# Kernel tuning notes

Measured on AMD Instinct MI355X. Metric: run time of the kernel, lower is better.

Reference implementation:

```python
import jax, jax.numpy as jnp
import numpy as np

D = 1024

def setup_inputs() -> dict:
    key = jax.random.key(0)
    ks = jax.random.split(key, 9)
    s = 1.0 / np.sqrt(D)
    x = jax.random.normal(ks[0], (4096, 8, D), dtype=jnp.float32)
    Wq = jax.random.uniform(ks[1], (D, D), jnp.float32, -s, s)
    bq = jax.random.uniform(ks[2], (D,), jnp.float32, -s, s)
    Wk = jax.random.uniform(ks[3], (D, D), jnp.float32, -s, s)
    bk = jax.random.uniform(ks[4], (D,), jnp.float32, -s, s)
    Wv = jax.random.uniform(ks[5], (D, D), jnp.float32, -s, s)
    bv = jax.random.uniform(ks[6], (D,), jnp.float32, -s, s)
    Wo = jax.random.uniform(ks[7], (D, D), jnp.float32, -s, s)
    bo = jax.random.uniform(ks[8], (D,), jnp.float32, -s, s)
    return {"x": x, "Wq": Wq, "bq": bq, "Wk": Wk, "bk": bk,
            "Wv": Wv, "bv": bv, "Wo": Wo, "bo": bo}

def reference(x, Wq, bq, Wk, bk, Wv, bv, Wo, bo):
    # x: (S, B, D) seq-first, matching torch module
    Q = jax.nn.elu(x @ Wq.T + bq) + 1.0  # (S,B,D)
    K = jax.nn.elu(x @ Wk.T + bk) + 1.0  # (S,B,D)
    V = x @ Wv.T + bv                    # (S,B,D)
    # KV = K^T V per batch: (B, D, D)
    KV = jnp.einsum('sbd,sbe->bde', K, V)
    # out = Q @ KV per batch, back to (S,B,D)
    out = jnp.einsum('sbd,bde->sbe', Q, KV)
    return out @ Wo.T + bo
```

## Files before the change

### kernel.cpp

```cpp
#include <hip/hip_runtime.h>


typedef __bf16 bf16;
typedef __attribute__((ext_vector_type(8))) __bf16 bf16x8;
typedef __attribute__((ext_vector_type(4))) __bf16 bf16x4;
typedef __attribute__((ext_vector_type(4))) float f32x4;

static constexpr int S = 4096;
static constexpr int B = 8;
static constexpr int D = 1024;
static constexpr int SB = S * B;
static constexpr long long NELEM = (long long)SB * D;

__device__ __forceinline__ void load_lds16(const bf16* g, void* l)
{
    __builtin_amdgcn_global_load_lds(
        (const __attribute__((address_space(1))) void*)g,
        (__attribute__((address_space(3))) void*)l, 16, 0, 0);
}

__global__ void cvt_f32_to_bf16(const float* __restrict__ in, bf16* __restrict__ out, int n)
{
    int i = (blockIdx.x * blockDim.x + threadIdx.x) * 4;
    int stride = gridDim.x * blockDim.x * 4;
    for (; i < n; i += stride) {
        float4 v = *(const float4*)(in + i);
        bf16x4 o;
        o[0] = (bf16)v.x; o[1] = (bf16)v.y; o[2] = (bf16)v.z; o[3] = (bf16)v.w;
        *(bf16x4*)(out + i) = o;
    }
}

__global__ void cvt_permute(const float* __restrict__ in, bf16* __restrict__ out)
{
    long long i = ((long long)blockIdx.x * blockDim.x + threadIdx.x) * 8;
    const long long stride = (long long)gridDim.x * blockDim.x * 8;
    for (; i < NELEM; i += stride) {
        const long long s = i >> 13;
        const long long r = i & 8191;
        const long long b = r >> 10;
        const long long d = r & 1023;
        float4 v0 = *(const float4*)(in + i);
        float4 v1 = *(const float4*)(in + i + 4);
        bf16x8 o;
        o[0] = (bf16)v0.x; o[1] = (bf16)v0.y; o[2] = (bf16)v0.z; o[3] = (bf16)v0.w;
        o[4] = (bf16)v1.x; o[5] = (bf16)v1.y; o[6] = (bf16)v1.z; o[7] = (bf16)v1.w;
        *(bf16x8*)(out + b * ((long long)S * D) + s * D + d) = o;
    }
}

__global__ __launch_bounds__(256) void cvt_transpose_1024(
    const float* __restrict__ in, bf16* __restrict__ out)
{
    __shared__ bf16 tile[64][72];
    const int e0 = blockIdx.y * 64;
    const int d0 = blockIdx.x * 64;
    const int t  = threadIdx.x;
    const int rl = t >> 3;
    const int c8 = (t & 7) * 8;
    #pragma unroll
    for (int p = 0; p < 2; ++p) {
        int r = rl + p * 32;
        float4 v0 = *(const float4*)(in + (long long)(e0 + r) * D + d0 + c8);
        float4 v1 = *(const float4*)(in + (long long)(e0 + r) * D + d0 + c8 + 4);
        tile[c8+0][r] = (bf16)v0.x; tile[c8+1][r] = (bf16)v0.y;
        tile[c8+2][r] = (bf16)v0.z; tile[c8+3][r] = (bf16)v0.w;
        tile[c8+4][r] = (bf16)v1.x; tile[c8+5][r] = (bf16)v1.y;
        tile[c8+6][r] = (bf16)v1.z; tile[c8+7][r] = (bf16)v1.w;
    }
    __syncthreads();
    #pragma unroll
    for (int p = 0; p < 2; ++p) {
        int dr = rl + p * 32;
        *(bf16x8*)(out + (long long)(d0 + dr) * D + e0 + c8) = *(bf16x8*)(&tile[dr][c8]);
    }
}

__global__ __launch_bounds__(256) void bvo_kernel(
    const float* __restrict__ Wo, const float* __restrict__ bv, float* __restrict__ bvo)
{
    const int row = blockIdx.x;
    const int t = threadIdx.x;
    float4 w = *(const float4*)(Wo + (long long)row * D + t * 4);
    float4 b = *(const float4*)(bv + t * 4);
    float s = w.x*b.x + w.y*b.y + w.z*b.z + w.w*b.w;
    __shared__ float red[256];
    red[t] = s; __syncthreads();
    for (int off = 128; off > 0; off >>= 1) {
        if (t < off) red[t] += red[t + off];
        __syncthreads();
    }
    if (t == 0) bvo[row] = red[0];
}

__global__ __launch_bounds__(256) void kv_add(const bf16* __restrict__ p, bf16* __restrict__ o)
{
    const long long DD = (long long)D * D;
    const int b = blockIdx.y;
    const long long i = ((long long)blockIdx.x * 256 + threadIdx.x) * 8;
    bf16x8 u = *(const bf16x8*)(p + (2 * b) * DD + i);
    bf16x8 v = *(const bf16x8*)(p + (2 * b + 1) * DD + i);
    bf16x8 r;
    #pragma unroll
    for (int j = 0; j < 8; ++j) r[j] = (bf16)((float)u[j] + (float)v[j]);
    *(bf16x8*)(o + b * DD + i) = r;
}

template<int BM, int BN, int WM, int WN, int EPI, int OUTF32, int BIASROW>
__global__ __launch_bounds__(WM * WN * 64, 2) void gemm_bt(
    const bf16* __restrict__ A, const bf16* __restrict__ Bm,
    const float* __restrict__ bias, void* __restrict__ Cout,
    int lda, int ldb, int ldc, int K,
    long long aBatch, long long bBatch, long long cBatch)
{
    constexpr int THREADS = WM * WN * 64;
    constexpr int WROWS = BM / WM, WCOLS = BN / WN;
    constexpr int MI = WROWS / 16, NI = WCOLS / 16;
    constexpr int ABYTES = BM * 64;
    constexpr int BBYTES = BN * 64;
    constexpr int BUF = ABYTES + BBYTES;

    __shared__ unsigned char smem[4 * BUF];

    const int tid  = threadIdx.x;
    const int lane = tid & 63;
    const int wave = tid >> 6;
    const int wr   = wave / WN;
    const int wc   = wave % WN;
    const int bz   = blockIdx.z;

    const int nx  = gridDim.x;
    const int bid = blockIdx.y * nx + blockIdx.x;
    const int cpx = (nx * gridDim.y) >> 3;
    const int swz = (bid & 7) * cpx + (bid >> 3);
    const long long m0 = (long long)(swz / nx) * BM;
    const long long n0 = (long long)(swz % nx) * BN;

    const bf16* Ab = A  + bz * aBatch + m0 * lda;
    const bf16* Bb = Bm + bz * bBatch + n0 * ldb;

    f32x4 acc[MI][NI] = {};
    const int NT = K >> 5;

    auto stage = [&](int t) {
        unsigned char* dst = smem + (t & 3) * BUF;
        const long long kk = (long long)t << 5;
        #pragma unroll
        for (int j = 0; j < 2; ++j) {
            const int g  = wave * 64 + lane + j * THREADS;
            const int gs = g ^ ((g >> 3) & 3);
            const int row = gs >> 2, col = (gs & 3) * 8;
            load_lds16(Ab + (long long)row * lda + kk + col,
                       dst + (wave * 64 + j * THREADS) * 16);
        }
        #pragma unroll
        for (int j = 0; j < 2; ++j) {
            const int g  = wave * 64 + lane + j * THREADS;
            const int gs = g ^ ((g >> 3) & 3);
            const int row = gs >> 2, col = (gs & 3) * 8;
            load_lds16(Bb + (long long)row * ldb + kk + col,
                       dst + ABYTES + (wave * 64 + j * THREADS) * 16);
        }
    };

    stage(0); stage(1); stage(2);

    const int ko2 = (lane >> 4) * 16;
    const int la15 = lane & 15;

    for (int t = 0; t < NT; ++t) {
        if (t + 2 < NT)      asm volatile("s_waitcnt vmcnt(8)" ::: "memory");
        else if (t + 1 < NT) asm volatile("s_waitcnt vmcnt(4)" ::: "memory");
        else                 asm volatile("s_waitcnt vmcnt(0)" ::: "memory");
        __builtin_amdgcn_s_barrier();
        asm volatile("" ::: "memory");

        if (t + 3 < NT) stage(t + 3);

        const unsigned char* buf = smem + (t & 3) * BUF;
        bf16x8 a[MI], b[NI];
        #pragma unroll
        for (int mi = 0; mi < MI; ++mi) {
            int ad = (wr * WROWS + mi * 16 + la15) * 64 + ko2;
            ad ^= ((ad >> 7) & 3) << 4;
            a[mi] = *(const bf16x8*)(buf + ad);
        }
        #pragma unroll
        for (int ni = 0; ni < NI; ++ni) {
            int ad = (wc * WCOLS + ni * 16 + la15) * 64 + ko2;
            ad ^= ((ad >> 7) & 3) << 4;
            b[ni] = *(const bf16x8*)(buf + ABYTES + ad);
        }

        __builtin_amdgcn_s_setprio(1);
        #pragma unroll
        for (int mi = 0; mi < MI; ++mi)
            #pragma unroll
            for (int ni = 0; ni < NI; ++ni)
                acc[mi][ni] = __builtin_amdgcn_mfma_f32_16x16x32_bf16(
                    a[mi], b[ni], acc[mi][ni], 0, 0, 0);
        __builtin_amdgcn_s_setprio(0);
    }

    const int crow = (lane >> 4) * 4;
    const int ccol = lane & 15;
    #pragma unroll
    for (int ni = 0; ni < NI; ++ni) {
        const long long c = n0 + wc * WCOLS + ni * 16 + ccol;
        float bcol = 0.0f;
        if (!BIASROW && bias) bcol = bias[c];
        #pragma unroll
        for (int mi = 0; mi < MI; ++mi) {
            const long long r0 = m0 + wr * WROWS + mi * 16 + crow;
            #pragma unroll
            for (int j = 0; j < 4; ++j) {
                float v = acc[mi][ni][j];
                v += BIASROW ? bias[r0 + j] : bcol;
                if (EPI == 1) v = (v > 0.0f) ? (v + 1.0f) : __expf(v);
                const long long idx = bz * cBatch + (r0 + j) * ldc + c;
                if (OUTF32) ((float*)Cout)[idx] = v;
                else        ((bf16*)Cout)[idx]  = (bf16)v;
            }
        }
    }
}

template<int EPI, int OUTF32, int BIASROW, int SPLITK, int GROUPN>
__global__ __launch_bounds__(512, 1) void gemm8p(
    const bf16* __restrict__ A, const bf16* __restrict__ Bm,
    const float* __restrict__ bias, void* __restrict__ Cout,
    int lda, int ldb, int ldc, int K,
    long long aBatch, long long bBatch, long long cBatch)
{
    __shared__ unsigned char smem[131072];

    const int tid  = threadIdx.x;
    const int lane = tid & 63;
    const int wave = tid >> 6;
    const int wr   = wave >> 2;
    const int wc   = wave & 3;
    const int bz    = blockIdx.z;
    const int batch = bz / SPLITK;
    const int kseg  = bz % SPLITK;

    const int nx  = gridDim.x;
    const int ny  = gridDim.y;
    const int bid = blockIdx.y * nx + blockIdx.x;
    const int cpx = (nx * ny) >> 3;
    const int swzb = (bid & 7) * cpx + (bid >> 3);
    long long m0, n0;
    if (GROUPN) { n0 = (long long)(swzb / ny) * 256; m0 = (long long)(swzb % ny) * 256; }
    else        { m0 = (long long)(swzb / nx) * 256; n0 = (long long)(swzb % nx) * 256; }

    const bf16* Ab = A  + batch * aBatch + m0 * lda + (long long)kseg * K;
    const bf16* Bb = Bm + batch * bBatch + n0 * ldb + (long long)kseg * K;

    const int sg = (lane & 3) ^ ((lane >> 3) & 3);
    const long long srow = wave * 32 + (lane >> 2);
    const bf16* srcA  = Ab + srow * lda + sg * 8;
    const bf16* srcA2 = srcA + 16 * (long long)lda;
    const bf16* srcB  = Bb + srow * ldb + sg * 8;
    const bf16* srcB2 = srcB + 16 * (long long)ldb;
    const int dstoff = wave * 2048;

    const int la15 = lane & 15;
    const int rsw  = (lane >> 4) ^ ((la15 >> 1) & 3);
    const int a16  = (wr * 128 + la15) * 4 + rsw;
    const int b16  = (wc * 64  + la15) * 4 + rsw;

    f32x4 acc[8][4] = {};
    const int NT = K >> 6;
    const int NI = NT >> 1;

    auto stageA = [&](int T, int kh) {
        const int reg = ((((T & 1) << 1) | kh) << 14);
        const long long kp = ((long long)T << 6) + (kh << 5);
        load_lds16(srcA  + kp, smem + reg + dstoff);
        load_lds16(srcA2 + kp, smem + reg + dstoff + 1024);
    };
    auto stageB = [&](int T, int kh) {
        const int reg = 65536 + ((((T & 1) << 1) | kh) << 14);
        const long long kp = ((long long)T << 6) + (kh << 5);
        load_lds16(srcB  + kp, smem + reg + dstoff);
        load_lds16(srcB2 + kp, smem + reg + dstoff + 1024);
    };

    stageB(0, 0); stageA(0, 0); stageB(0, 1); stageA(0, 1);
    stageB(1, 0); stageA(1, 0); stageB(1, 1);
    asm volatile("s_waitcnt vmcnt(6)" ::: "memory");

    bf16x8 bfr[4];
    for (int i = 0; i < NI; ++i) {
        const int t = 2 * i;
        const bool nl = (i + 1 < NI);
        #pragma unroll
        for (int p = 0; p < 8; ++p) {
            const int ks  = (p >> 1) & 1;
            const int ch  = p & 1;
            const int buf = p >> 2;
            const int regA = ((buf << 1) | ks) << 14;
            const int regB = 65536 + regA;

            __builtin_amdgcn_s_barrier();
            __builtin_amdgcn_sched_barrier(0);

            bf16x8 afr[4];
            if (ch == 0) {
                #pragma unroll
                for (int ni = 0; ni < 4; ++ni)
                    bfr[ni] = *(const bf16x8*)(smem + regB + (b16 + ni * 64) * 16);
            }
            #pragma unroll
            for (int m4 = 0; m4 < 4; ++m4)
                afr[m4] = *(const bf16x8*)(smem + regA + (a16 + (ch * 4 + m4) * 64) * 16);

            if      (p == 0) stageA(t + 1, 1);
            else if (p == 1) { if (t + 2 < NT) stageB(t + 2, 0); }
            else if (p == 2) { if (t + 2 < NT) stageA(t + 2, 0); }
            else if (p == 3) { if (t + 2 < NT) stageB(t + 2, 1); }
            else if (p == 4) { if (t + 2 < NT) stageA(t + 2, 1); }
            else if (p == 5) { if (t + 3 < NT) stageB(t + 3, 0); }
            else if (p == 6) { if (t + 3 < NT) stageA(t + 3, 0); }
            else             { if (t + 3 < NT) stageB(t + 3, 1); }

            if (p == 3) {
                if (nl) asm volatile("s_waitcnt vmcnt(6)" ::: "memory");
                else    asm volatile("s_waitcnt vmcnt(0)" ::: "memory");
            } else if (p == 7) {
                if (nl) asm volatile("s_waitcnt vmcnt(6)" ::: "memory");
            }

            __builtin_amdgcn_s_setprio(1);
            #pragma unroll
            for (int m4 = 0; m4 < 4; ++m4)
                #pragma unroll
                for (int ni = 0; ni < 4; ++ni)
                    acc[ch * 4 + m4][ni] = __builtin_amdgcn_mfma_f32_16x16x32_bf16(
                        afr[m4], bfr[ni], acc[ch * 4 + m4][ni], 0, 0, 0);
            __builtin_amdgcn_s_setprio(0);
        }
    }

    const bool doElu = (EPI == 1) || (EPI == 2 && m0 < 1024);
    const long long cb = (long long)bz * cBatch;
    const int crow = (lane >> 4) * 4;

    if constexpr (OUTF32 != 0) {
        float* lt = (float*)smem;
        #pragma unroll
        for (int q = 0; q < 4; ++q) {
            __builtin_amdgcn_s_barrier();
            __builtin_amdgcn_sched_barrier(0);
            if (wr == (q >> 1)) {
                #pragma unroll
                for (int m4 = 0; m4 < 4; ++m4) {
                    const int mi = (q & 1) * 4 + m4;
                    const int lrow = m4 * 16 + crow;
                    const long long r0 = m0 + q * 64 + lrow;
                    #pragma unroll
                    for (int ni = 0; ni < 4; ++ni) {
                        const int lcol = wc * 64 + ni * 16 + la15;
                        float bb = 0.0f;
                        if (!BIASROW && bias) bb = bias[n0 + lcol];
                        #pragma unroll
                        for (int j = 0; j < 4; ++j) {
                            float v = acc[mi][ni][j] + (BIASROW ? bias[r0 + j] : bb);
                            if (doElu) v = (v > 0.0f) ? (v + 1.0f) : __expf(v);
                            lt[(lrow + j) * 260 + lcol] = v;
                        }
                    }
                }
            }
            __builtin_amdgcn_s_barrier();
            #pragma unroll
            for (int it = 0; it < 8; ++it) {
                const int chk = it * 512 + tid;
                const int r   = chk >> 6;
                const int g   = chk & 63;
                float4 v = *(const float4*)(lt + r * 260 + g * 4);
                *(float4*)((float*)Cout + cb + (m0 + q * 64 + r) * ldc + n0 + g * 4) = v;
            }
        }
    } else {
        bf16* lt = (bf16*)smem;
        #pragma unroll
        for (int half = 0; half < 2; ++half) {
            __builtin_amdgcn_s_barrier();
            __builtin_amdgcn_sched_barrier(0);
            if (wr == half) {
                #pragma unroll
                for (int mi = 0; mi < 8; ++mi) {
                    const int lrow = mi * 16 + crow;
                    const long long r0 = m0 + half * 128 + lrow;
                    #pragma unroll
                    for (int ni = 0; ni < 4; ++ni) {
                        const int lcol = wc * 64 + ni * 16 + la15;
                        float bb = 0.0f;
                        if (!BIASROW && bias) bb = bias[n0 + lcol];
                        #pragma unroll
                        for (int j = 0; j < 4; ++j) {
                            float v = acc[mi][ni][j] + (BIASROW ? bias[r0 + j] : bb);
                            if (doElu) v = (v > 0.0f) ? (v + 1.0f) : __expf(v);
                            lt[(lrow + j) * 264 + lcol] = (bf16)v;
                        }
                    }
                }
            }
            __builtin_amdgcn_s_barrier();
            #pragma unroll
            for (int it = 0; it < 8; ++it) {
                const int chk = it * 512 + tid;
                const int m   = chk >> 5;
                const int nof = (chk & 31) * 8;
                bf16x8 v = *(const bf16x8*)(lt + m * 264 + nof);
                *(bf16x8*)((bf16*)Cout + cb + (m0 + half * 128 + m) * ldc + n0 + nof) = v;
            }
        }
    }
}

extern "C" void kernel_launch(void* const* d_in, const int* in_sizes, int n_in,
                              void* d_out, int out_size, void* d_ws, size_t ws_size,
                              hipStream_t stream)
{
    const float* x  = (const float*)d_in[0];
    const float* Wq = (const float*)d_in[1];
    const float* bq = (const float*)d_in[2];
    const float* Wk = (const float*)d_in[3];
    const float* bk = (const float*)d_in[4];
    const float* Wv = (const float*)d_in[5];
    const float* bv = (const float*)d_in[6];
    const float* Wo = (const float*)d_in[7];
    const float* bo = (const float*)d_in[8];
    float* out = (float*)d_out;

    char* ws = (char*)d_ws;
    if (ws_size < (size_t)159383552) return;
    bf16*  xbp  = (bf16*)(ws + 0);
    bf16*  part = (bf16*)(ws + 67108864);
    bf16*  Qb   = (bf16*)(ws + 67108864);
    bf16*  wvT  = (bf16*)(ws + 134217728);
    float* bkvo = (float*)(ws + 134217728 + 2097152);
    bf16*  KVo  = (bf16*)(ws + 134217728);
    bf16*  wqb  = (bf16*)(ws + 150994944);
    bf16*  wob  = wqb + 1048576;
    bf16*  wkvo = wob + 1048576;
    bf16*  KVb  = (bf16*)d_out;

    const long long SD = (long long)S * D;

    cvt_permute<<<8192, 256, 0, stream>>>(x, xbp);
    cvt_f32_to_bf16<<<1024, 256, 0, stream>>>(Wq, wqb, D * D);
    cvt_f32_to_bf16<<<1024, 256, 0, stream>>>(Wo, wob, D * D);
    cvt_f32_to_bf16<<<1024, 256, 0, stream>>>(Wk, wkvo, D * D);
    cvt_transpose_1024<<<dim3(16, 16), 256, 0, stream>>>(Wv, wvT);
    bvo_kernel<<<1024, 256, 0, stream>>>(Wo, bv, bkvo + 1024);
    hipMemcpyAsync(bkvo, bk, D * sizeof(float), hipMemcpyDeviceToDevice, stream);

    gemm_bt<128, 128, 2, 2, 0, 0, 0><<<dim3(8, 8, 1), 256, 0, stream>>>(
        wob, wvT, nullptr, wkvo + (long long)1024 * 1024, D, D, D, D, 0, 0, 0);

    gemm8p<2, 0, 1, 1, 1><<<dim3(16, 8, 8), 512, 0, stream>>>(
        wkvo, xbp, bkvo, KVb, D, D, S, D,
        0, SD, (long long)2048 * S);

    gemm8p<0, 0, 0, 2, 0><<<dim3(4, 4, 16), 512, 0, stream>>>(
        KVb + (long long)1024 * S, KVb, nullptr, part, S, S, D, 2048,
        (long long)2048 * S, (long long)2048 * S, (long long)D * D);

    kv_add<<<dim3(512, 8), 256, 0, stream>>>(part, KVo);

    gemm8p<1, 0, 0, 1, 0><<<dim3(4, 16, 8), 512, 0, stream>>>(
        xbp, wqb, bq, Qb, D, D, D, D, SD, 0, SD);

    gemm8p<0, 1, 0, 1, 0><<<dim3(4, 16, 8), 512, 0, stream>>>(
        Qb, KVo, bo, out, D, D, B * D, D,
        SD, (long long)D * D, (long long)D);
}
```

Baseline: 487.2 us.

## Add 128x128-tile GEMM kernel with two-per-CU occupancy for projection GEMMs

Adds a new 256-thread GEMM kernel with 128x128 output tiles, a double-buffered direct-to-LDS load pipeline, an XOR-swizzled LDS layout and a grouped block swizzle. It replaces the larger 512-thread gemm8p tiles in the K/V projection, Q projection and output projection, launching four times as many blocks. The aim is better occupancy (launch bounds of 2 blocks per CU) and load balance across CUs, at the cost of less operand reuse per tile and more global traffic.

```diff
diff --git a/kernel.cpp b/kernel.cpp
--- a/kernel.cpp
+++ b/kernel.cpp
@@ -419,6 +419,174 @@
     }
 }
 
+template<int EPI, int OUTF32, int BIASROW, int GROUPN>
+__global__ __launch_bounds__(256, 2) void gemm_r128(
+    const bf16* __restrict__ A, const bf16* __restrict__ Bm,
+    const float* __restrict__ bias, void* __restrict__ Cout,
+    int lda, int ldb, int ldc, int K,
+    long long aBatch, long long bBatch, long long cBatch)
+{
+    __shared__ unsigned char smem[32768];
+
+    const int tid  = threadIdx.x;
+    const int lane = tid & 63;
+    const int wave = tid >> 6;
+    const int wr   = wave >> 1;
+    const int wc   = wave & 1;
+    const int bz   = blockIdx.z;
+
+    const int nx  = gridDim.x;
+    const int ny  = gridDim.y;
+    const int bid = blockIdx.y * nx + blockIdx.x;
+    const int cpx = (nx * ny) >> 3;
+    const int swzb = (bid & 7) * cpx + (bid >> 3);
+    long long m0, n0;
+    if (GROUPN) { n0 = (long long)(swzb / ny) * 128; m0 = (long long)(swzb % ny) * 128; }
+    else        { m0 = (long long)(swzb / nx) * 128; n0 = (long long)(swzb % nx) * 128; }
+
+    const bf16* Ab = A  + bz * aBatch + m0 * lda;
+    const bf16* Bb = Bm + bz * bBatch + n0 * ldb;
+
+    const int g0row = tid >> 2;
+    const int g0ks  = (tid & 3) ^ (g0row & 3);
+    const int g1row = (tid + 256) >> 2;
+    const int g1ks  = (tid & 3) ^ (g1row & 3);
+    const bf16* sA0 = Ab + (long long)g0row * lda + g0ks * 8;
+    const bf16* sA1 = Ab + (long long)g1row * lda + g1ks * 8;
+    const bf16* sB0 = Bb + (long long)g0row * ldb + g0ks * 8;
+    const bf16* sB1 = Bb + (long long)g1row * ldb + g1ks * 8;
+    const int dst0 = tid * 16;
+
+    auto stage = [&](int T, int cur) {
+        const long long kp = (long long)T << 5;
+        unsigned char* base = smem + cur * 16384;
+        load_lds16(sA0 + kp, base + dst0);
+        load_lds16(sA1 + kp, base + 4096 + dst0);
+        load_lds16(sB0 + kp, base + 8192 + dst0);
+        load_lds16(sB1 + kp, base + 8192 + 4096 + dst0);
+    };
+
+    const int la15 = lane & 15;
+    const int hi   = lane >> 4;
+    const int gsw  = hi ^ (la15 & 3);
+    const int abase = (wr * 64 + la15) * 4 + gsw;
+    const int bbase = (wc * 64 + la15) * 4 + gsw;
+
+    f32x4 acc[4][4] = {};
+    const int NT = K >> 5;
+
+    stage(0, 0); stage(1, 1);
+    asm volatile("s_waitcnt vmcnt(4)" ::: "memory");
+    __builtin_amdgcn_s_barrier();
+
+    for (int t = 0; t < NT; ++t) {
+        const int cur = t & 1;
+        const unsigned char* Abase = smem + cur * 16384;
+        const unsigned char* Bbase = Abase + 8192;
+
+        bf16x8 a[4], b[4];
+        #pragma unroll
+        for (int ni = 0; ni < 4; ++ni)
+            b[ni] = *(const bf16x8*)(Bbase + (bbase + ni * 64) * 16);
+        #pragma unroll
+        for (int mi = 0; mi < 4; ++mi)
+            a[mi] = *(const bf16x8*)(Abase + (abase + mi * 64) * 16);
+
+        asm volatile("s_waitcnt lgkmcnt(0)" ::: "memory");
+        __builtin_amdgcn_s_barrier();
+
+        if (t + 2 < NT) stage(t + 2, cur);
+
+        __builtin_amdgcn_s_setprio(1);
+        #pragma unroll
+        for (int mi = 0; mi < 4; ++mi)
+            #pragma unroll
+            for (int ni = 0; ni < 4; ++ni)
+                acc[mi][ni] = __builtin_amdgcn_mfma_f32_16x16x32_bf16(
+                    a[mi], b[ni], acc[mi][ni], 0, 0, 0);
+        __builtin_amdgcn_s_setprio(0);
+
+        if (t + 2 < NT)      asm volatile("s_waitcnt vmcnt(4)" ::: "memory");
+        else if (t + 1 < NT) asm volatile("s_waitcnt vmcnt(0)" ::: "memory");
+        __builtin_amdgcn_s_barrier();
+    }
+
+    const bool doElu = (EPI == 1) || (EPI == 2 && m0 < 1024);
+    const long long cb = (long long)bz * cBatch;
+    const int crow = hi * 4;
+
+    if constexpr (OUTF32 != 0) {
+        float* lt = (float*)smem;
+        #pragma unroll
+        for (int q = 0; q < 4; ++q) {
+            __builtin_amdgcn_s_barrier();
+            if (wr == (q >> 1)) {
+                #pragma unroll
+                for (int f = 0; f < 2; ++f) {
+                    const int mi = (q & 1) * 2 + f;
+                    const int lrow = f * 16 + crow;
+                    const long long r0 = m0 + q * 32 + lrow;
+                    #pragma unroll
+                    for (int ni = 0; ni < 4; ++ni) {
+                        const int lcol = wc * 64 + ni * 16 + la15;
+                        float bb = 0.0f;
+                        if (!BIASROW && bias) bb = bias[n0 + lcol];
+                        #pragma unroll
+                        for (int j = 0; j < 4; ++j) {
+                            float v = acc[mi][ni][j] + (BIASROW ? bias[r0 + j] : bb);
+                            if (doElu) v = (v > 0.0f) ? (v + 1.0f) : __expf(v);
+                            lt[(lrow + j) * 132 + lcol] = v;
+                        }
+                    }
+                }
+            }
+            __builtin_amdgcn_s_barrier();
+            #pragma unroll
+            for (int it = 0; it < 4; ++it) {
+                const int chk = it * 256 + tid;
+                const int r   = chk >> 5;
+                const int g   = chk & 31;
+                float4 v = *(const float4*)(lt + r * 132 + g * 4);
+                *(float4*)((float*)Cout + cb + (m0 + q * 32 + r) * ldc + n0 + g * 4) = v;
+            }
+        }
+    } else {
+        bf16* lt = (bf16*)smem;
+        #pragma unroll
+        for (int h = 0; h < 2; ++h) {
+            __builtin_amdgcn_s_barrier();
+            if (wr == h) {
+                #pragma unroll
+                for (int mi = 0; mi < 4; ++mi) {
+                    const int lrow = mi * 16 + crow;
+                    const long long r0 = m0 + h * 64 + lrow;
+                    #pragma unroll
+                    for (int ni = 0; ni < 4; ++ni) {
+                        const int lcol = wc * 64 + ni * 16 + la15;
+                        float bb = 0.0f;
+                        if (!BIASROW && bias) bb = bias[n0 + lcol];
+                        #pragma unroll
+                        for (int j = 0; j < 4; ++j) {
+                            float v = acc[mi][ni][j] + (BIASROW ? bias[r0 + j] : bb);
+                            if (doElu) v = (v > 0.0f) ? (v + 1.0f) : __expf(v);
+                            lt[(lrow + j) * 136 + lcol] = (bf16)v;
+                        }
+                    }
+                }
+            }
+            __builtin_amdgcn_s_barrier();
+            #pragma unroll
+            for (int it = 0; it < 4; ++it) {
+                const int chk = it * 256 + tid;
+                const int m   = chk >> 4;
+                const int nof = (chk & 15) * 8;
+                bf16x8 v = *(const bf16x8*)(lt + m * 136 + nof);
+                *(bf16x8*)((bf16*)Cout + cb + (m0 + h * 64 + m) * ldc + n0 + nof) = v;
+            }
+        }
+    }
+}
+
 extern "C" void kernel_launch(void* const* d_in, const int* in_sizes, int n_in,
                               void* d_out, int out_size, void* d_ws, size_t ws_size,
                               hipStream_t stream)
@@ -460,7 +628,7 @@
     gemm_bt<128, 128, 2, 2, 0, 0, 0><<<dim3(8, 8, 1), 256, 0, stream>>>(
         wob, wvT, nullptr, wkvo + (long long)1024 * 1024, D, D, D, D, 0, 0, 0);
 
-    gemm8p<2, 0, 1, 1, 1><<<dim3(16, 8, 8), 512, 0, stream>>>(
+    gemm_r128<2, 0, 1, 1><<<dim3(32, 16, 8), 256, 0, stream>>>(
         wkvo, xbp, bkvo, KVb, D, D, S, D,
         0, SD, (long long)2048 * S);
 
@@ -470,10 +638,10 @@
 
     kv_add<<<dim3(512, 8), 256, 0, stream>>>(part, KVo);
 
-    gemm8p<1, 0, 0, 1, 0><<<dim3(4, 16, 8), 512, 0, stream>>>(
+    gemm_r128<1, 0, 0, 0><<<dim3(8, 32, 8), 256, 0, stream>>>(
         xbp, wqb, bq, Qb, D, D, D, D, SD, 0, SD);
 
-    gemm8p<0, 1, 0, 1, 0><<<dim3(4, 16, 8), 512, 0, stream>>>(
+    gemm_r128<0, 1, 0, 0><<<dim3(8, 32, 8), 256, 0, stream>>>(
         Qb, KVo, bo, out, D, D, B * D, D,
         SD, (long long)D * D, (long long)D);
 }
```

New measurement: 517.2 us. 6.1% more time.
